# Kernel optimization log

Hardware: AMD Instinct MI355X
Metric: run time of the kernel (lower is better)

The kernel has to match this reference:

```python
import jax, jax.numpy as jnp
import numpy as np

H = 32      # query heads
KV = 8      # kv heads
D = 128     # head_dim
HID = 4096
S = 4       # num sequences
L = 1024    # tokens per sequence
N = S * L   # total tokens
EPS = 1e-6
THETA = 10000.0
GROUPS = H // KV


def setup_inputs() -> dict:
    key = jax.random.key(0)
    ks = jax.random.split(key, 12)
    def w(k, shape, std):
        return jax.random.normal(k, shape, dtype=jnp.float32) * std
    return {
        "hidden": w(ks[0], (N, HID), 1.0),
        "mu_prev": w(ks[1], (N, HID), 1.0),
        "positions": jnp.tile(jnp.arange(L, dtype=jnp.int32), S),
        "Wq": w(ks[2], (H * D, HID), HID ** -0.5),
        "Wk": w(ks[3], (KV * D, HID), HID ** -0.5),
        "Wv": w(ks[4], (KV * D, HID), HID ** -0.5),
        "Wo": w(ks[5], (HID, H * D), (H * D) ** -0.5),
        "Wmq": w(ks[6], (H * D, HID), 0.01),
        "Wmk": w(ks[7], (KV * D, HID), 0.01),
        "Wmv": w(ks[8], (KV * D, HID), 0.01),
        "q_norm_w": jnp.ones((D,), jnp.float32),
        "k_norm_w": jnp.ones((D,), jnp.float32),
    }


def _rmsnorm(x, w):
    var = jnp.mean(jnp.square(x), axis=-1, keepdims=True)
    return x * jax.lax.rsqrt(var + EPS) * w


def _rope_cos_sin(positions):
    inv_freq = 1.0 / (THETA ** (jnp.arange(0, D, 2, dtype=jnp.float32) / D))  # [D/2]
    freqs = positions.astype(jnp.float32)[:, None] * inv_freq[None, :]        # [N, D/2]
    emb = jnp.concatenate([freqs, freqs], axis=-1)                            # [N, D]
    return jnp.cos(emb), jnp.sin(emb)


def _rotate_half(x):
    x1, x2 = jnp.split(x, 2, axis=-1)
    return jnp.concatenate([-x2, x1], axis=-1)


def _apply_rotary(x, cos, sin):
    # x: [N, h, D]; cos/sin: [N, D]
    return x * cos[:, None, :] + _rotate_half(x) * sin[:, None, :]


def reference(hidden, mu_prev, positions, Wq, Wk, Wv, Wo, Wmq, Wmk, Wmv, q_norm_w, k_norm_w):
    # QKV projections + mu-bias fusion
    q = hidden @ Wq.T + mu_prev @ Wmq.T     # [N, H*D]
    k = hidden @ Wk.T + mu_prev @ Wmk.T     # [N, KV*D]
    v = hidden @ Wv.T + mu_prev @ Wmv.T     # [N, KV*D]
    q = q.reshape(N, H, D)
    k = k.reshape(N, KV, D)
    v = v.reshape(N, KV, D)
    # QK RMSNorm
    q = _rmsnorm(q, q_norm_w)
    k = _rmsnorm(k, k_norm_w)
    # RoPE
    cos, sin = _rope_cos_sin(positions)
    q = _apply_rotary(q, cos, sin)
    k = _apply_rotary(k, cos, sin)
    # GQA: expand kv heads to match q heads
    k = jnp.repeat(k, GROUPS, axis=1)       # [N, H, D]
    v = jnp.repeat(v, GROUPS, axis=1)
    # Varlen causal attention: equal-length seqs -> batched [S, L, H, D]
    qs = q.reshape(S, L, H, D)
    ks = k.reshape(S, L, H, D)
    vs = v.reshape(S, L, H, D)
    scale = 1.0 / np.sqrt(D)
    scores = jnp.einsum("slhd,smhd->shlm", qs, ks) * scale   # [S, H, L, L]
    causal = jnp.tril(jnp.ones((L, L), dtype=bool))
    scores = jnp.where(causal, scores, jnp.finfo(scores.dtype).min)
    probs = jax.nn.softmax(scores, axis=-1)
    out = jnp.einsum("shlm,smhd->slhd", probs, vs)           # [S, L, H, D]
    out = out.reshape(N, H * D)
    return out @ Wo.T                                         # [N, HID]
```

## Files before the change

### kernel.cpp

```cpp
#include <hip/hip_runtime.h>
#include <hip/hip_bf16.h>
#include <stdint.h>

#define DEV static __device__ __forceinline__

typedef __bf16 bf16_t;
typedef __bf16 bf16x8 __attribute__((ext_vector_type(8)));
typedef __bf16 bf16x4 __attribute__((ext_vector_type(4)));
typedef float  f32x4  __attribute__((ext_vector_type(4)));


DEV void gload_lds16(const void* g, void* l) {
  __builtin_amdgcn_global_load_lds(
      (__attribute__((address_space(1))) void*)(uintptr_t)(g),
      (__attribute__((address_space(3))) void*)(uintptr_t)(l),
      16, 0, 0);
}

#define BARRIER() asm volatile("s_barrier" ::: "memory")
#define MFMA16(a, b, c) __builtin_amdgcn_mfma_f32_16x16x32_bf16((a), (b), (c), 0, 0, 0)

DEV void pack_pair_chunk(const float* __restrict__ A, const float* __restrict__ B,
                         bf16_t* __restrict__ dst, size_t i) {
  size_t r = i >> 10, c = i & 1023;
  float4 va = ((const float4*)A)[i];
  float4 vb = ((const float4*)B)[i];
  bf16x4 oa = {(bf16_t)va.x, (bf16_t)va.y, (bf16_t)va.z, (bf16_t)va.w};
  bf16x4 ob = {(bf16_t)vb.x, (bf16_t)vb.y, (bf16_t)vb.z, (bf16_t)vb.w};
  ((bf16x4*)dst)[r * 2048 + c] = oa;
  ((bf16x4*)dst)[r * 2048 + 1024 + c] = ob;
}

__global__ void k_pack_all(const float* __restrict__ hidden, const float* __restrict__ mu,
                           const float* __restrict__ Wq, const float* __restrict__ Wmq,
                           const float* __restrict__ Wk, const float* __restrict__ Wmk,
                           const float* __restrict__ Wv, const float* __restrict__ Wmv,
                           const float* __restrict__ Wo,
                           bf16_t* __restrict__ Xb, bf16_t* __restrict__ Wqkv,
                           bf16_t* __restrict__ Wob) {
  const size_t t0 = 4194304, t1 = 8388608, t2 = 9437184, t3 = 10485760, t4 = 14680064;
  size_t stride = (size_t)gridDim.x * blockDim.x;
  for (size_t i = (size_t)blockIdx.x * blockDim.x + threadIdx.x; i < t4; i += stride) {
    if (i < t0) {
      pack_pair_chunk(hidden, mu, Xb, i);
    } else if (i < t1) {
      pack_pair_chunk(Wq, Wmq, Wqkv, i - t0);
    } else if (i < t2) {
      pack_pair_chunk(Wk, Wmk, Wqkv + (size_t)4096 * 8192, i - t1);
    } else if (i < t3) {
      pack_pair_chunk(Wv, Wmv, Wqkv + (size_t)5120 * 8192, i - t2);
    } else {
      size_t j = i - t3;
      float4 v = ((const float4*)Wo)[j];
      bf16x4 o = {(bf16_t)v.x, (bf16_t)v.y, (bf16_t)v.z, (bf16_t)v.w};
      ((bf16x4*)Wob)[j] = o;
    }
  }
}

template<typename CT, int NSPLIT>
__global__ __launch_bounds__(512, 2) void k_gemm256(
    const bf16_t* __restrict__ A, const bf16_t* __restrict__ B,
    CT* __restrict__ C, int M, int N, int Kfull) {
  __shared__ __align__(16) char lds[131072];
  const int tid = threadIdx.x, lane = tid & 63, wid = tid >> 6;
  const int l15 = lane & 15, lhi = lane >> 4;
  const int wr = wid >> 2, wc = wid & 3;
  const int bid = blockIdx.x, nwg = gridDim.x;
  const int cpx = nwg >> 3;
  const int swz = (bid & 7) * cpx + (bid >> 3);
  const int nbm = M >> 8;
  const int tiles = nbm * (N >> 8);
  const int ks = (NSPLIT > 1) ? (swz / tiles) : 0;
  const int t  = (NSPLIT > 1) ? (swz % tiles) : swz;
  const int bm = t % nbm, bn = t / nbm;
  const int Kloop = Kfull / NSPLIT;
  const int nkt = Kloop >> 6;

  const size_t rowK = (size_t)Kfull * 2;
  const size_t kbase = (size_t)ks * Kloop * 2;
  const int off0 = wid * 1024 + lane * 16, off1 = off0 + 8192;
  const int r0 = off0 >> 7, r1 = off1 >> 7;
  const int c0 = ((off0 >> 4) & 7) ^ (r0 & 7);
  const int c1 = ((off1 >> 4) & 7) ^ (r1 & 7);
  const char* sA0 = (const char*)A + ((size_t)bm * 256 + r0) * rowK + kbase + c0 * 16;
  const char* sA1 = (const char*)A + ((size_t)bm * 256 + r1) * rowK + kbase + c1 * 16;
  const char* sB0 = (const char*)B + ((size_t)bn * 256 + r0) * rowK + kbase + c0 * 16;
  const char* sB1 = (const char*)B + ((size_t)bn * 256 + r1) * rowK + kbase + c1 * 16;
  const size_t hst = (size_t)128 * rowK;

  enum { A0S = 0, A1S = 16384, A2S = 32768, A3S = 49152,
         B0S = 65536, B1S = 81920, B2S = 98304, B3S = 114688 };

#define STG(slot, pa, pb, off) do { \
    gload_lds16((pa) + (off), lds + (slot) + wid * 1024); \
    gload_lds16((pb) + (off), lds + (slot) + 8192 + wid * 1024); } while (0)

  const bf16_t* Ae = (const bf16_t*)(lds + A0S + wr * 16384);
  const bf16_t* Be = (const bf16_t*)(lds + B0S + (wc >> 1) * 16384);
  const bf16_t* Ao = (const bf16_t*)(lds + A2S + wr * 16384);
  const bf16_t* Bo = (const bf16_t*)(lds + B2S + (wc >> 1) * 16384);
  const int bro = (wc & 1) * 64;

  f32x4 acc[8][4] = {};
  bf16x8 a[4][2], b[4][2];
  const int xr = l15 & 7;
  const int ck0 = (lhi ^ xr) * 8;
  const int ck1 = ((4 + lhi) ^ xr) * 8;

#define RD_A(base, rb) do { _Pragma("unroll") \
    for (int mi = 0; mi < 4; ++mi) { \
      const int ro = ((rb) + mi * 16 + l15) * 64; \
      a[mi][0] = *(const bf16x8*)((base) + ro + ck0); \
      a[mi][1] = *(const bf16x8*)((base) + ro + ck1); } } while (0)
#define RD_B(base) do { _Pragma("unroll") \
    for (int n = 0; n < 4; ++n) { \
      const int ro = (bro + n * 16 + l15) * 64; \
      b[n][0] = *(const bf16x8*)((base) + ro + ck0); \
      b[n][1] = *(const bf16x8*)((base) + ro + ck1); } } while (0)
#define MM(qm, qn) do { _Pragma("unroll") \
    for (int mi = 0; mi < 4; ++mi) { _Pragma("unroll") \
      for (int ni = 0; ni < 2; ++ni) { \
        f32x4 t_ = acc[(qm) * 4 + mi][(qn) * 2 + ni]; \
        t_ = MFMA16(a[mi][0], b[(qn) * 2 + ni][0], t_); \
        t_ = MFMA16(a[mi][1], b[(qn) * 2 + ni][1], t_); \
        acc[(qm) * 4 + mi][(qn) * 2 + ni] = t_; } } } while (0)
#define PRIO_MM(qm, qn) do { __builtin_amdgcn_s_setprio(1); MM(qm, qn); \
    __builtin_amdgcn_s_setprio(0); } while (0)
#define LGKM0() asm volatile("s_waitcnt lgkmcnt(0)" ::: "memory")

  STG(B0S, sB0, sB1, 0);
  STG(B1S, sB0, sB1, hst);
  STG(A0S, sA0, sA1, 0);
  STG(A1S, sA0, sA1, hst);
  STG(B2S, sB0, sB1, 128);
  STG(B3S, sB0, sB1, 128 + hst);
  STG(A2S, sA0, sA1, 128);
  STG(A3S, sA0, sA1, 128 + hst);
  asm volatile("s_waitcnt vmcnt(8)" ::: "memory");
  BARRIER();

  size_t g = 0;
  for (int ktp = 0; ktp < nkt / 2 - 1; ++ktp) {
    RD_A(Ae, 0); RD_B(Be);
    LGKM0();
    BARRIER();
    STG(B0S, sB0, sB1, g + 256);
    STG(B1S, sB0, sB1, g + 256 + hst);
    PRIO_MM(0, 0);
    PRIO_MM(0, 1);
    RD_A(Ae, 64);
    LGKM0();
    BARRIER();
    STG(A0S, sA0, sA1, g + 256);
    STG(A1S, sA0, sA1, g + 256 + hst);
    PRIO_MM(1, 0);
    PRIO_MM(1, 1);
    asm volatile("s_waitcnt vmcnt(8)" ::: "memory");
    BARRIER();
    RD_A(Ao, 0); RD_B(Bo);
    LGKM0();
    BARRIER();
    STG(B2S, sB0, sB1, g + 384);
    STG(B3S, sB0, sB1, g + 384 + hst);
    PRIO_MM(0, 0);
    PRIO_MM(0, 1);
    RD_A(Ao, 64);
    LGKM0();
    BARRIER();
    STG(A2S, sA0, sA1, g + 384);
    STG(A3S, sA0, sA1, g + 384 + hst);
    PRIO_MM(1, 0);
    PRIO_MM(1, 1);
    asm volatile("s_waitcnt vmcnt(8)" ::: "memory");
    BARRIER();
    g += 256;
  }
  RD_A(Ae, 0); RD_B(Be);
  PRIO_MM(0, 0);
  PRIO_MM(0, 1);
  RD_A(Ae, 64);
  PRIO_MM(1, 0);
  PRIO_MM(1, 1);
  asm volatile("s_waitcnt vmcnt(0)" ::: "memory");
  BARRIER();
  RD_A(Ao, 0); RD_B(Bo);
  PRIO_MM(0, 0);
  PRIO_MM(0, 1);
  RD_A(Ao, 64);
  PRIO_MM(1, 0);
  PRIO_MM(1, 1);

  CT* Cp = C + (size_t)ks * M * N;
#pragma unroll
  for (int m = 0; m < 8; ++m) {
    const int row0 = bm * 256 + wr * 128 + m * 16 + 4 * lhi;
#pragma unroll
    for (int n = 0; n < 4; ++n) {
      const int col = bn * 256 + wc * 64 + n * 16 + l15;
#pragma unroll
      for (int i = 0; i < 4; ++i)
        Cp[(size_t)(row0 + i) * N + col] = (CT)acc[m][n][i];
    }
  }
#undef STG
#undef RD_A
#undef RD_B
#undef MM
#undef PRIO_MM
#undef LGKM0
}

__global__ __launch_bounds__(256) void k_norm_rope(
    const bf16_t* __restrict__ qkvA, const bf16_t* __restrict__ qkvB,
    const int* __restrict__ pos,
    const float* __restrict__ qw, const float* __restrict__ kw,
    bf16_t* __restrict__ Q, bf16_t* __restrict__ Kk, bf16_t* __restrict__ V) {
  const int w = blockIdx.x * 4 + (threadIdx.x >> 6);
  const int lane = threadIdx.x & 63;
  const int n = w / 48, slot = w % 48;
  const bf16_t* rowA = qkvA + (size_t)n * 6144;
  const bf16_t* rowB = qkvB + (size_t)n * 6144;
  if (slot >= 40) {
    const int h2 = slot - 40;
    const int c = 5120 + h2 * 128 + lane;
    float x0 = (float)rowA[c] + (float)rowB[c];
    float x1 = (float)rowA[c + 64] + (float)rowB[c + 64];
    bf16_t* dst = V + ((size_t)n * 8 + h2) * 128;
    dst[lane] = (bf16_t)x0;
    dst[lane + 64] = (bf16_t)x1;
    return;
  }
  const bool isq = slot < 32;
  const int h = isq ? slot : slot - 32;
  const int coff = (isq ? h * 128 : 4096 + h * 128) + lane;
  float x0 = (float)rowA[coff] + (float)rowB[coff];
  float x1 = (float)rowA[coff + 64] + (float)rowB[coff + 64];
  float ss = x0 * x0 + x1 * x1;
#pragma unroll
  for (int m = 32; m; m >>= 1) ss += __shfl_xor(ss, m, 64);
  const float inv = rsqrtf(ss * (1.0f / 128.0f) + 1e-6f);
  const float* wgt = isq ? qw : kw;
  float y0 = x0 * inv * wgt[lane];
  float y1 = x1 * inv * wgt[lane + 64];
  const float ang = (float)pos[n] * expf((float)lane * -0.14391156608f);
  float sn, cs;
  sincosf(ang, &sn, &cs);
  float o0 = y0 * cs - y1 * sn;
  float o1 = y1 * cs + y0 * sn;
  bf16_t* dst = isq ? (Q + ((size_t)n * 32 + h) * 128) : (Kk + ((size_t)n * 8 + h) * 128);
  dst[lane] = (bf16_t)o0;
  dst[lane + 64] = (bf16_t)o1;
}

__global__ __launch_bounds__(256) void k_vt(const bf16_t* __restrict__ V,
                                            bf16_t* __restrict__ Vt) {
  __shared__ bf16_t T[64][136];
  const int blk = blockIdx.x;
  const int tt = blk & 15, kvh = (blk >> 4) & 7, s = blk >> 7;
  const int tok0 = tt * 64;
  const int tid = threadIdx.x;
#pragma unroll
  for (int k = 0; k < 4; ++k) {
    const int item = tid + k * 256;
    const int tok = item >> 4, d0 = (item & 15) * 8;
    bf16x8 v = *(const bf16x8*)(V + ((size_t)(s * 1024 + tok0 + tok) * 8 + kvh) * 128 + d0);
    *(bf16x8*)(&T[tok][d0]) = v;
  }
  __syncthreads();
#pragma unroll
  for (int k = 0; k < 4; ++k) {
    const int item = tid + k * 256;
    const int d = item & 127, oct = item >> 7;
    bf16x8 o;
#pragma unroll
    for (int j = 0; j < 8; ++j) o[j] = T[oct * 8 + j][d];
    *(bf16x8*)(Vt + ((size_t)((s * 8 + kvh) * 128 + d)) * 1024 + tok0 + oct * 8) = o;
  }
}

__global__ __launch_bounds__(256, 2) void k_attn(
    const bf16_t* __restrict__ Q, const bf16_t* __restrict__ Kk,
    const bf16_t* __restrict__ Vt, bf16_t* __restrict__ O) {
  __shared__ __align__(16) bf16_t Ks[2][64 * 128];
  __shared__ __align__(16) bf16_t Ps[4][32 * 72];
  const int b = blockIdx.x;
  const int x = b & 7, y = b >> 3;
  const int h = x * 4 + ((y >> 3) & 3);
  const int qb = 7 - (y & 7);
  const int s = y >> 5;
  const int kvh = h >> 2;
  const int tid = threadIdx.x, lane = tid & 63, wid = tid >> 6;
  const int l15 = lane & 15, lhi = lane >> 4;

  bf16x8 qf[2][4];
  {
    const int qrow = qb * 128 + wid * 32;
#pragma unroll
    for (int mt = 0; mt < 2; mt++) {
      const size_t base = ((size_t)(s * 1024 + qrow + mt * 16 + l15) * 32 + h) * 128;
#pragma unroll
      for (int kc = 0; kc < 4; kc++)
        qf[mt][kc] = *(const bf16x8*)(Q + base + kc * 32 + 8 * lhi);
    }
  }
  const bf16_t* Vtb = Vt + (size_t)((s * 8 + kvh) * 128) * 1024;

  f32x4 of[2][8] = {};
  float mx[2][4], li[2][4];
#pragma unroll
  for (int mt = 0; mt < 2; mt++)
#pragma unroll
    for (int i = 0; i < 4; i++) { mx[mt][i] = -1e30f; li[mt][i] = 0.f; }

  const int ktiles = (qb + 1) * 2;

  const int so = wid * 4096;
#define STAGE_K(kt_, buf_) do { _Pragma("unroll") \
    for (int c = 0; c < 4; ++c) { \
      const int o = so + c * 1024 + lane * 16; \
      const int krow = o >> 8; \
      const int cs = ((o >> 4) & 15) ^ (krow & 7); \
      const char* src = (const char*)(Kk + \
          ((size_t)(s * 1024 + (kt_) * 64 + krow) * 8 + kvh) * 128) + cs * 16; \
      gload_lds16(src, (char*)&Ks[buf_][0] + so + c * 1024); \
    } } while (0)

  STAGE_K(0, 0);
  asm volatile("s_waitcnt vmcnt(0)" ::: "memory");
  BARRIER();

  for (int kt = 0; kt < ktiles; kt++) {
    const int kv0 = kt * 64;
    const int buf = kt & 1;
    if (kt + 1 < ktiles) STAGE_K(kt + 1, buf ^ 1);

    f32x4 sf[2][4] = {};
#pragma unroll
    for (int kc = 0; kc < 4; kc++) {
      bf16x8 kf[4];
#pragma unroll
      for (int n = 0; n < 4; n++) {
        const int krow = n * 16 + l15;
        const int ci = (kc * 4 + lhi) ^ (krow & 7);
        kf[n] = *(const bf16x8*)(&Ks[buf][0] + krow * 128 + ci * 8);
      }
#pragma unroll
      for (int mt = 0; mt < 2; mt++)
#pragma unroll
        for (int n = 0; n < 4; n++)
          sf[mt][n] = MFMA16(qf[mt][kc], kf[n], sf[mt][n]);
    }

    const bool masked = (kt >= 2 * qb);
    const float scale = 0.08838834764831845f;
    float pv[2][4][4];
#pragma unroll
    for (int mt = 0; mt < 2; mt++) {
#pragma unroll
      for (int i = 0; i < 4; i++) {
        float rm = -1e30f;
#pragma unroll
        for (int n = 0; n < 4; n++) {
          float sv = sf[mt][n][i] * scale;
          if (masked) {
            const int kvg = kv0 + n * 16 + l15;
            const int qg = qb * 128 + wid * 32 + mt * 16 + 4 * lhi + i;
            if (kvg > qg) sv = -1e30f;
          }
          pv[mt][n][i] = sv;
          rm = fmaxf(rm, sv);
        }
#pragma unroll
        for (int mm = 1; mm < 16; mm <<= 1) rm = fmaxf(rm, __shfl_xor(rm, mm, 64));
        const float nm = fmaxf(mx[mt][i], rm);
        float ts = 0.f;
#pragma unroll
        for (int n = 0; n < 4; n++) {
          float e = __expf(pv[mt][n][i] - nm);
          pv[mt][n][i] = e;
          ts += e;
        }
#pragma unroll
        for (int mm = 1; mm < 16; mm <<= 1) ts += __shfl_xor(ts, mm, 64);
        const float al = __expf(mx[mt][i] - nm);
        li[mt][i] = li[mt][i] * al + ts;
        mx[mt][i] = nm;
#pragma unroll
        for (int n = 0; n < 8; n++) of[mt][n][i] *= al;
      }
    }

    bf16_t* myP = &Ps[wid][0];
#pragma unroll
    for (int mt = 0; mt < 2; mt++)
#pragma unroll
      for (int n = 0; n < 4; n++)
#pragma unroll
        for (int i = 0; i < 4; i++)
          myP[(mt * 16 + 4 * lhi + i) * 72 + n * 16 + l15] = (bf16_t)pv[mt][n][i];

#pragma unroll
    for (int kc = 0; kc < 2; kc++) {
      bf16x8 pf[2];
#pragma unroll
      for (int mt = 0; mt < 2; mt++)
        pf[mt] = *(const bf16x8*)(myP + (mt * 16 + l15) * 72 + kc * 32 + 8 * lhi);
#pragma unroll
      for (int n = 0; n < 8; n++) {
        const int d = n * 16 + l15;
        bf16x8 vf = *(const bf16x8*)(Vtb + (size_t)d * 1024 + kv0 + kc * 32 + 8 * lhi);
#pragma unroll
        for (int mt = 0; mt < 2; mt++)
          of[mt][n] = MFMA16(pf[mt], vf, of[mt][n]);
      }
    }

    if (kt + 1 < ktiles) {
      asm volatile("s_waitcnt vmcnt(0)" ::: "memory");
      BARRIER();
    }
  }
#undef STAGE_K

#pragma unroll
  for (int mt = 0; mt < 2; mt++) {
#pragma unroll
    for (int i = 0; i < 4; i++) {
      const float invl = 1.0f / li[mt][i];
      const int tokrow = qb * 128 + wid * 32 + mt * 16 + 4 * lhi + i;
      bf16_t* dst = O + (size_t)(s * 1024 + tokrow) * 4096 + h * 128;
#pragma unroll
      for (int n = 0; n < 8; n++)
        dst[n * 16 + l15] = (bf16_t)(of[mt][n][i] * invl);
    }
  }
}

extern "C" void kernel_launch(void* const* d_in, const int* in_sizes, int n_in,
                              void* d_out, int out_size, void* d_ws, size_t ws_size,
                              hipStream_t stream) {
  const float* hidden = (const float*)d_in[0];
  const float* mu     = (const float*)d_in[1];
  const int*   pos    = (const int*)d_in[2];
  const float* Wq  = (const float*)d_in[3];
  const float* Wk  = (const float*)d_in[4];
  const float* Wv  = (const float*)d_in[5];
  const float* Wo  = (const float*)d_in[6];
  const float* Wmq = (const float*)d_in[7];
  const float* Wmk = (const float*)d_in[8];
  const float* Wmv = (const float*)d_in[9];
  const float* qw  = (const float*)d_in[10];
  const float* kw  = (const float*)d_in[11];
  float* out = (float*)d_out;
  char* ws = (char*)d_ws;

  if (ws_size < 301989888u) return;

  bf16_t* Wqkv = (bf16_t*)(ws);
  bf16_t* Wob  = (bf16_t*)(ws + 100663296);
  bf16_t* Xb   = (bf16_t*)(ws + 134217728);
  bf16_t* Qb   = (bf16_t*)(ws + 134217728);
  bf16_t* Kb   = (bf16_t*)(ws + 167772160);
  bf16_t* Vb   = (bf16_t*)(ws + 176160768);
  bf16_t* VtG  = (bf16_t*)(ws + 184549376);
  bf16_t* qkvA = (bf16_t*)(ws + 201326592);
  bf16_t* qkvB = (bf16_t*)(ws + 251658240);
  bf16_t* Ob   = (bf16_t*)(ws + 201326592);

  k_pack_all<<<2048, 256, 0, stream>>>(hidden, mu, Wq, Wmq, Wk, Wmk, Wv, Wmv, Wo,
                                       Xb, Wqkv, Wob);
  k_gemm256<bf16_t, 2><<<768, 512, 0, stream>>>(Xb, Wqkv, qkvA, 4096, 6144, 8192);
  k_norm_rope<<<49152, 256, 0, stream>>>(qkvA, qkvB, pos, qw, kw, Qb, Kb, Vb);
  k_vt<<<512, 256, 0, stream>>>(Vb, VtG);
  k_attn<<<1024, 256, 0, stream>>>(Qb, Kb, VtG, Ob);
  k_gemm256<float, 1><<<256, 512, 0, stream>>>(Ob, Wob, out, 4096, 4096, 4096);
}
```

Baseline: 775.1 us.

## Replace split-K 256x256 GEMM with 128x256 triple-buffered GEMM, drop split-K partials

Replaces the 512-thread 256x256 GEMM with a 256-thread 128x256 tile kernel that uses K-steps of 32 and a three-stage LDS ring buffer with a single barrier per iteration. The QKV projection no longer uses split-K, so the two bf16 partial outputs and their sum in the norm/RoPE kernel go away, and the output projection launches twice as many blocks. The goal is to cut partial-sum traffic, keep more workgroups resident with smaller LDS use, and overlap loads better. The cost is lower per-block reuse (128-row A tiles) and more barriers per unit of K.

```diff
diff --git a/kernel.cpp b/kernel.cpp
--- a/kernel.cpp
+++ b/kernel.cpp
@@ -58,184 +58,113 @@
   }
 }
 
-template<typename CT, int NSPLIT>
-__global__ __launch_bounds__(512, 2) void k_gemm256(
+template<typename CT>
+__global__ __launch_bounds__(256, 2) void k_gemm(
     const bf16_t* __restrict__ A, const bf16_t* __restrict__ B,
     CT* __restrict__ C, int M, int N, int Kfull) {
-  __shared__ __align__(16) char lds[131072];
+  __shared__ __align__(16) char lds[73728];
   const int tid = threadIdx.x, lane = tid & 63, wid = tid >> 6;
   const int l15 = lane & 15, lhi = lane >> 4;
-  const int wr = wid >> 2, wc = wid & 3;
+  const int wm = wid >> 1, wn = wid & 1;
   const int bid = blockIdx.x, nwg = gridDim.x;
   const int cpx = nwg >> 3;
   const int swz = (bid & 7) * cpx + (bid >> 3);
-  const int nbm = M >> 8;
-  const int tiles = nbm * (N >> 8);
-  const int ks = (NSPLIT > 1) ? (swz / tiles) : 0;
-  const int t  = (NSPLIT > 1) ? (swz % tiles) : swz;
-  const int bm = t % nbm, bn = t / nbm;
-  const int Kloop = Kfull / NSPLIT;
-  const int nkt = Kloop >> 6;
+  const int nbm = M >> 7;
+  const int bm = swz % nbm, bn = swz / nbm;
+  const int nkt = Kfull >> 5;
 
   const size_t rowK = (size_t)Kfull * 2;
-  const size_t kbase = (size_t)ks * Kloop * 2;
-  const int off0 = wid * 1024 + lane * 16, off1 = off0 + 8192;
-  const int r0 = off0 >> 7, r1 = off1 >> 7;
-  const int c0 = ((off0 >> 4) & 7) ^ (r0 & 7);
-  const int c1 = ((off1 >> 4) & 7) ^ (r1 & 7);
-  const char* sA0 = (const char*)A + ((size_t)bm * 256 + r0) * rowK + kbase + c0 * 16;
-  const char* sA1 = (const char*)A + ((size_t)bm * 256 + r1) * rowK + kbase + c1 * 16;
-  const char* sB0 = (const char*)B + ((size_t)bn * 256 + r0) * rowK + kbase + c0 * 16;
-  const char* sB1 = (const char*)B + ((size_t)bn * 256 + r1) * rowK + kbase + c1 * 16;
-  const size_t hst = (size_t)128 * rowK;
-
-  enum { A0S = 0, A1S = 16384, A2S = 32768, A3S = 49152,
-         B0S = 65536, B1S = 81920, B2S = 98304, B3S = 114688 };
-
-#define STG(slot, pa, pb, off) do { \
-    gload_lds16((pa) + (off), lds + (slot) + wid * 1024); \
-    gload_lds16((pb) + (off), lds + (slot) + 8192 + wid * 1024); } while (0)
-
-  const bf16_t* Ae = (const bf16_t*)(lds + A0S + wr * 16384);
-  const bf16_t* Be = (const bf16_t*)(lds + B0S + (wc >> 1) * 16384);
-  const bf16_t* Ao = (const bf16_t*)(lds + A2S + wr * 16384);
-  const bf16_t* Bo = (const bf16_t*)(lds + B2S + (wc >> 1) * 16384);
-  const int bro = (wc & 1) * 64;
-
-  f32x4 acc[8][4] = {};
-  bf16x8 a[4][2], b[4][2];
-  const int xr = l15 & 7;
-  const int ck0 = (lhi ^ xr) * 8;
-  const int ck1 = ((4 + lhi) ^ xr) * 8;
-
-#define RD_A(base, rb) do { _Pragma("unroll") \
-    for (int mi = 0; mi < 4; ++mi) { \
-      const int ro = ((rb) + mi * 16 + l15) * 64; \
-      a[mi][0] = *(const bf16x8*)((base) + ro + ck0); \
-      a[mi][1] = *(const bf16x8*)((base) + ro + ck1); } } while (0)
-#define RD_B(base) do { _Pragma("unroll") \
-    for (int n = 0; n < 4; ++n) { \
-      const int ro = (bro + n * 16 + l15) * 64; \
-      b[n][0] = *(const bf16x8*)((base) + ro + ck0); \
-      b[n][1] = *(const bf16x8*)((base) + ro + ck1); } } while (0)
-#define MM(qm, qn) do { _Pragma("unroll") \
-    for (int mi = 0; mi < 4; ++mi) { _Pragma("unroll") \
-      for (int ni = 0; ni < 2; ++ni) { \
-        f32x4 t_ = acc[(qm) * 4 + mi][(qn) * 2 + ni]; \
-        t_ = MFMA16(a[mi][0], b[(qn) * 2 + ni][0], t_); \
-        t_ = MFMA16(a[mi][1], b[(qn) * 2 + ni][1], t_); \
-        acc[(qm) * 4 + mi][(qn) * 2 + ni] = t_; } } } while (0)
-#define PRIO_MM(qm, qn) do { __builtin_amdgcn_s_setprio(1); MM(qm, qn); \
-    __builtin_amdgcn_s_setprio(0); } while (0)
-#define LGKM0() asm volatile("s_waitcnt lgkmcnt(0)" ::: "memory")
-
-  STG(B0S, sB0, sB1, 0);
-  STG(B1S, sB0, sB1, hst);
-  STG(A0S, sA0, sA1, 0);
-  STG(A1S, sA0, sA1, hst);
-  STG(B2S, sB0, sB1, 128);
-  STG(B3S, sB0, sB1, 128 + hst);
-  STG(A2S, sA0, sA1, 128);
-  STG(A3S, sA0, sA1, 128 + hst);
-  asm volatile("s_waitcnt vmcnt(8)" ::: "memory");
+  const int srow = tid >> 2;
+  const int scs = (tid & 3) ^ (srow & 3);
+  const char* sA = (const char*)A + ((size_t)bm * 128 + srow) * rowK + scs * 16;
+  const char* sB = (const char*)B + ((size_t)bn * 256 + srow) * rowK + scs * 16;
+  const size_t r64 = (size_t)64 * rowK;
+
+  char* buf0 = lds;
+  char* buf1 = lds + 24576;
+  char* buf2 = lds + 49152;
+
+#define STG(buf, kb) do { \
+    gload_lds16(sA + (kb),            (buf) + tid * 16); \
+    gload_lds16(sA + r64 + (kb),      (buf) + 4096 + tid * 16); \
+    gload_lds16(sB + (kb),            (buf) + 8192 + tid * 16); \
+    gload_lds16(sB + r64 + (kb),      (buf) + 12288 + tid * 16); \
+    gload_lds16(sB + 2 * r64 + (kb),  (buf) + 16384 + tid * 16); \
+    gload_lds16(sB + 3 * r64 + (kb),  (buf) + 20480 + tid * 16); } while (0)
+
+  const int fch = (lhi ^ (l15 & 3)) << 4;
+  int a_off[4], b_off[8];
+#pragma unroll
+  for (int mi = 0; mi < 4; ++mi) a_off[mi] = (wm * 64 + mi * 16 + l15) * 64 + fch;
+#pragma unroll
+  for (int ni = 0; ni < 8; ++ni) b_off[ni] = 8192 + (wn * 128 + ni * 16 + l15) * 64 + fch;
+
+  f32x4 acc[4][8] = {};
+
+  STG(buf0, 0);
+  STG(buf1, 64);
+  asm volatile("s_waitcnt vmcnt(6)" ::: "memory");
   BARRIER();
 
-  size_t g = 0;
-  for (int ktp = 0; ktp < nkt / 2 - 1; ++ktp) {
-    RD_A(Ae, 0); RD_B(Be);
-    LGKM0();
+  char* cur = buf0;
+  char* nxt = buf1;
+  char* stg = buf2;
+  for (int t = 0; t < nkt; ++t) {
+    const int tn = (t + 2 < nkt) ? (t + 2) : (nkt - 1);
+    STG(stg, (size_t)tn * 64);
+    bf16x8 a[4], b[8];
+#pragma unroll
+    for (int mi = 0; mi < 4; ++mi) a[mi] = *(const bf16x8*)(cur + a_off[mi]);
+#pragma unroll
+    for (int ni = 0; ni < 8; ++ni) b[ni] = *(const bf16x8*)(cur + b_off[ni]);
+    asm volatile("s_waitcnt lgkmcnt(0)" ::: "memory");
+    __builtin_amdgcn_s_setprio(1);
+#pragma unroll
+    for (int mi = 0; mi < 4; ++mi)
+#pragma unroll
+      for (int ni = 0; ni < 8; ++ni)
+        acc[mi][ni] = MFMA16(a[mi], b[ni], acc[mi][ni]);
+    __builtin_amdgcn_s_setprio(0);
+    asm volatile("s_waitcnt vmcnt(6)" ::: "memory");
     BARRIER();
-    STG(B0S, sB0, sB1, g + 256);
-    STG(B1S, sB0, sB1, g + 256 + hst);
-    PRIO_MM(0, 0);
-    PRIO_MM(0, 1);
-    RD_A(Ae, 64);
-    LGKM0();
-    BARRIER();
-    STG(A0S, sA0, sA1, g + 256);
-    STG(A1S, sA0, sA1, g + 256 + hst);
-    PRIO_MM(1, 0);
-    PRIO_MM(1, 1);
-    asm volatile("s_waitcnt vmcnt(8)" ::: "memory");
-    BARRIER();
-    RD_A(Ao, 0); RD_B(Bo);
-    LGKM0();
-    BARRIER();
-    STG(B2S, sB0, sB1, g + 384);
-    STG(B3S, sB0, sB1, g + 384 + hst);
-    PRIO_MM(0, 0);
-    PRIO_MM(0, 1);
-    RD_A(Ao, 64);
-    LGKM0();
-    BARRIER();
-    STG(A2S, sA0, sA1, g + 384);
-    STG(A3S, sA0, sA1, g + 384 + hst);
-    PRIO_MM(1, 0);
-    PRIO_MM(1, 1);
-    asm volatile("s_waitcnt vmcnt(8)" ::: "memory");
-    BARRIER();
-    g += 256;
-  }
-  RD_A(Ae, 0); RD_B(Be);
-  PRIO_MM(0, 0);
-  PRIO_MM(0, 1);
-  RD_A(Ae, 64);
-  PRIO_MM(1, 0);
-  PRIO_MM(1, 1);
-  asm volatile("s_waitcnt vmcnt(0)" ::: "memory");
-  BARRIER();
-  RD_A(Ao, 0); RD_B(Bo);
-  PRIO_MM(0, 0);
-  PRIO_MM(0, 1);
-  RD_A(Ao, 64);
-  PRIO_MM(1, 0);
-  PRIO_MM(1, 1);
-
-  CT* Cp = C + (size_t)ks * M * N;
-#pragma unroll
-  for (int m = 0; m < 8; ++m) {
-    const int row0 = bm * 256 + wr * 128 + m * 16 + 4 * lhi;
-#pragma unroll
-    for (int n = 0; n < 4; ++n) {
-      const int col = bn * 256 + wc * 64 + n * 16 + l15;
+    char* tmp = cur; cur = nxt; nxt = stg; stg = tmp;
+  }
+
+#pragma unroll
+  for (int mi = 0; mi < 4; ++mi) {
+    const int row0 = bm * 128 + wm * 64 + mi * 16 + 4 * lhi;
+#pragma unroll
+    for (int ni = 0; ni < 8; ++ni) {
+      const int col = bn * 256 + wn * 128 + ni * 16 + l15;
 #pragma unroll
       for (int i = 0; i < 4; ++i)
-        Cp[(size_t)(row0 + i) * N + col] = (CT)acc[m][n][i];
+        C[(size_t)(row0 + i) * N + col] = (CT)acc[mi][ni][i];
     }
   }
 #undef STG
-#undef RD_A
-#undef RD_B
-#undef MM
-#undef PRIO_MM
-#undef LGKM0
 }
 
 __global__ __launch_bounds__(256) void k_norm_rope(
-    const bf16_t* __restrict__ qkvA, const bf16_t* __restrict__ qkvB,
-    const int* __restrict__ pos,
+    const bf16_t* __restrict__ qkv, const int* __restrict__ pos,
     const float* __restrict__ qw, const float* __restrict__ kw,
     bf16_t* __restrict__ Q, bf16_t* __restrict__ Kk, bf16_t* __restrict__ V) {
   const int w = blockIdx.x * 4 + (threadIdx.x >> 6);
   const int lane = threadIdx.x & 63;
   const int n = w / 48, slot = w % 48;
-  const bf16_t* rowA = qkvA + (size_t)n * 6144;
-  const bf16_t* rowB = qkvB + (size_t)n * 6144;
+  const bf16_t* row = qkv + (size_t)n * 6144;
   if (slot >= 40) {
     const int h2 = slot - 40;
     const int c = 5120 + h2 * 128 + lane;
-    float x0 = (float)rowA[c] + (float)rowB[c];
-    float x1 = (float)rowA[c + 64] + (float)rowB[c + 64];
     bf16_t* dst = V + ((size_t)n * 8 + h2) * 128;
-    dst[lane] = (bf16_t)x0;
-    dst[lane + 64] = (bf16_t)x1;
+    dst[lane] = row[c];
+    dst[lane + 64] = row[c + 64];
     return;
   }
   const bool isq = slot < 32;
   const int h = isq ? slot : slot - 32;
   const int coff = (isq ? h * 128 : 4096 + h * 128) + lane;
-  float x0 = (float)rowA[coff] + (float)rowB[coff];
-  float x1 = (float)rowA[coff + 64] + (float)rowB[coff + 64];
+  float x0 = (float)row[coff];
+  float x1 = (float)row[coff + 64];
   float ss = x0 * x0 + x1 * x1;
 #pragma unroll
   for (int m = 32; m; m >>= 1) ss += __shfl_xor(ss, m, 64);
@@ -464,15 +393,14 @@
   bf16_t* Kb   = (bf16_t*)(ws + 167772160);
   bf16_t* Vb   = (bf16_t*)(ws + 176160768);
   bf16_t* VtG  = (bf16_t*)(ws + 184549376);
-  bf16_t* qkvA = (bf16_t*)(ws + 201326592);
-  bf16_t* qkvB = (bf16_t*)(ws + 251658240);
+  bf16_t* qkv  = (bf16_t*)(ws + 201326592);
   bf16_t* Ob   = (bf16_t*)(ws + 201326592);
 
   k_pack_all<<<2048, 256, 0, stream>>>(hidden, mu, Wq, Wmq, Wk, Wmk, Wv, Wmv, Wo,
                                        Xb, Wqkv, Wob);
-  k_gemm256<bf16_t, 2><<<768, 512, 0, stream>>>(Xb, Wqkv, qkvA, 4096, 6144, 8192);
-  k_norm_rope<<<49152, 256, 0, stream>>>(qkvA, qkvB, pos, qw, kw, Qb, Kb, Vb);
+  k_gemm<bf16_t><<<768, 256, 0, stream>>>(Xb, Wqkv, qkv, 4096, 6144, 8192);
+  k_norm_rope<<<49152, 256, 0, stream>>>(qkv, pos, qw, kw, Qb, Kb, Vb);
   k_vt<<<512, 256, 0, stream>>>(Vb, VtG);
   k_attn<<<1024, 256, 0, stream>>>(Qb, Kb, VtG, Ob);
-  k_gemm256<float, 1><<<256, 512, 0, stream>>>(Ob, Wob, out, 4096, 4096, 4096);
-}
+  k_gemm<float><<<512, 256, 0, stream>>>(Ob, Wob, out, 4096, 4096, 4096);
+}
```

After: 880.1 us. 1.14x slower.
